# Kernel tuning notes

Measured on AMD Instinct MI355X. Metric: run time of the kernel, lower is better.

Reference implementation:

```python
import jax, jax.numpy as jnp
import numpy as np

EPS_LN = 1e-5
EPS_VAR = 1e-4
GAMMA = 1.0
H, D = 8, 64  # heads, dim_head
DIM = 512
QG, N = 8, 1024  # query groups, tokens


def layernorm(x, g, b):
    mu = x.mean(-1, keepdims=True)
    var = ((x - mu) ** 2).mean(-1, keepdims=True)
    return (x - mu) * jax.lax.rsqrt(var + EPS_LN) * g + b


def setup_inputs() -> dict:
    key = jax.random.key(0)
    ks = jax.random.split(key, 12)
    s_in = 1.0 / np.sqrt(DIM)
    s_p1 = 1.0 / np.sqrt(2 * D)
    s_p2 = 1.0 / np.sqrt(D)
    return {
        "q": jax.random.normal(ks[0], (QG, N, DIM), jnp.float32),
        "k": jax.random.normal(ks[1], (QG, N, DIM), jnp.float32),
        "v": jax.random.normal(ks[2], (QG, N, DIM), jnp.float32),
        "ln_g": jnp.ones((DIM,), jnp.float32),
        "ln_b": jnp.zeros((DIM,), jnp.float32),
        "w_in": jax.random.uniform(ks[3], (DIM, H * D), jnp.float32, -s_in, s_in),
        "p_w1": jax.random.uniform(ks[4], (2 * D, D), jnp.float32, -s_p1, s_p1),
        "p_b1": jax.random.uniform(ks[5], (D,), jnp.float32, -s_p1, s_p1),
        "p_ln_g": jnp.ones((D,), jnp.float32),
        "p_ln_b": jnp.zeros((D,), jnp.float32),
        "p_w2": jax.random.uniform(ks[6], (D, 1), jnp.float32, -s_p2, s_p2),
        "p_b2": jax.random.uniform(ks[7], (1,), jnp.float32, -s_p2, s_p2),
        "w_out": jax.random.uniform(ks[8], (H * D, DIM), jnp.float32, -s_in, s_in),
        "b_out": jax.random.uniform(ks[9], (DIM,), jnp.float32, -s_in, s_in),
    }


def variance_term(E):
    flat = E.reshape(-1, E.shape[-1])  # [h*q*n, d]
    std = jnp.sqrt(jnp.var(flat, axis=0, ddof=1) + EPS_VAR)
    return jnp.maximum(GAMMA - std, 0.0).mean()


def reference(q, k, v, ln_g, ln_b, w_in, p_w1, p_b1, p_ln_g, p_ln_b, p_w2, p_b2, w_out, b_out):
    def proj(t):
        x = layernorm(t, ln_g, ln_b) @ w_in  # [q, n, h*d]
        return jnp.transpose(x.reshape(QG, N, H, D), (2, 0, 1, 3))  # [h, q, n, d]

    f_q, f_k, f_v = proj(q), proj(k), proj(v)

    # cosine-distance scores
    dots = jnp.einsum("hqnd,hqmd->hqnm", f_q, f_k)
    nq = jnp.linalg.norm(f_q, axis=-1)  # [h, q, n]
    nk = jnp.linalg.norm(f_k, axis=-1)  # [h, q, n]
    cos = dots / (nq[..., :, None] * nk[..., None, :])

    # covariance scores (mean-centered over feature dim)
    q_c = f_q - f_q.mean(-1, keepdims=True)
    k_c = f_k - f_k.mean(-1, keepdims=True)
    cov = jnp.einsum("hqnd,hqmd->hqnm", q_c, k_c) / D

    # dynamic per-head mixing weight via small MLP gate
    v_pen = variance_term(f_q) + variance_term(f_k)
    qg = f_q.mean((1, 2))  # [h, d]
    kg = f_k.mean((1, 2))  # [h, d]
    x = jnp.concatenate([qg, kg], -1)  # [h, 2d]
    h1 = jax.nn.relu(layernorm(x @ p_w1 + p_b1, p_ln_g, p_ln_b))
    w = jax.nn.sigmoid(h1 @ p_w2 + p_b2)  # [h, 1]
    w = (w / (1.0 + v_pen)).reshape(H, 1, 1, 1)

    mixed = (1.0 - w) * cos + w * cov  # [h, q, n, n] (no softmax)
    out = jnp.einsum("hqnm,hqmd->hqnd", mixed, f_v)
    out = jnp.transpose(out, (1, 2, 0, 3)).reshape(QG, N, H * D)  # 'h q n d -> q n (h d)'
    return out @ w_out + b_out
```

## Files before the change

### kernel.cpp

```cpp
#include <hip/hip_runtime.h>
#include <cstdint>


typedef unsigned short u16;
typedef unsigned int u32;
typedef __attribute__((ext_vector_type(8))) unsigned short u16x8;
typedef __attribute__((ext_vector_type(4))) unsigned short u16x4;
typedef __attribute__((ext_vector_type(8))) short short8;
typedef __attribute__((ext_vector_type(4))) float floatx4;

#define WS_XBF     0LL
#define WS_OATT    4194304LL
#define WS_WPT     6291456LL
#define WS_WOT     6422528LL
#define WS_U       6553600LL
#define WS_CB      6554112LL
#define WS_LNST    6554624LL
#define WS_FQ      6603776LL
#define WS_FKTS    8700928LL
#define WS_FKTC    10798080LL
#define WS_FVT     12895232LL
#define WS_INVNQ   14992384LL
#define WS_INVNK   15057920LL
#define WS_QMEAN   15123456LL
#define WS_KMEAN   15188992LL
#define WS_COLP    15254528LL
#define WS_WGATE   15385600LL
#define WS_WTF32   15385664LL
#define WS_GSUM    15385664LL
#define WS_MTB     15385664LL
#define WS_CTB     15516736LL
#define WS_COLC    15647808LL

__device__ __forceinline__ float wsum(float v) {
#pragma unroll
    for (int m = 32; m; m >>= 1) v += __shfl_xor(v, m, 64);
    return v;
}
__device__ __forceinline__ u16 f2bf(float f) {
    u32 u = __float_as_uint(f);
    u32 r = u + 0x7fffu + ((u >> 16) & 1u);
    return (u16)(r >> 16);
}
__device__ __forceinline__ float bf2f(u16 u) {
    return __uint_as_float(((u32)u) << 16);
}

__global__ __launch_bounds__(256) void k_lnstats(
    const float* __restrict__ q, const float* __restrict__ k,
    const float* __restrict__ v, float* __restrict__ ws) {
    int wid = threadIdx.x >> 6, lane = threadIdx.x & 63;
    int row = blockIdx.x * 4 + wid;
    int t = row >> 13, r = row & 8191;
    const float* src = (t == 0) ? q : ((t == 1) ? k : v);
    const float4* p = (const float4*)(src + (size_t)r * 512) + lane * 2;
    float4 a = p[0], b = p[1];
    u16x8 o;
    o[0] = f2bf(a.x); o[1] = f2bf(a.y); o[2] = f2bf(a.z); o[3] = f2bf(a.w);
    o[4] = f2bf(b.x); o[5] = f2bf(b.y); o[6] = f2bf(b.z); o[7] = f2bf(b.w);
    *(u16x8*)((u16*)(ws + WS_XBF) + (size_t)row * 512 + lane * 8) = o;
    float s = a.x + a.y + a.z + a.w + b.x + b.y + b.z + b.w;
    float ss = a.x * a.x + a.y * a.y + a.z * a.z + a.w * a.w +
               b.x * b.x + b.y * b.y + b.z * b.z + b.w * b.w;
    s = wsum(s); ss = wsum(ss);
    if (lane == 0) {
        float mu = s * (1.f / 512.f);
        float var = ss * (1.f / 512.f) - mu * mu;
        ws[WS_LNST + (size_t)row * 2] = mu;
        ws[WS_LNST + (size_t)row * 2 + 1] = rsqrtf(var + 1e-5f);
    }
}

template <int SCALE>
__global__ __launch_bounds__(256) void k_prep_t(
    const float* __restrict__ W, const float* __restrict__ g,
    u16* __restrict__ Tb, float* __restrict__ Tf) {
    __shared__ float tile[64][65];
    int k0 = blockIdx.x * 64, j0 = blockIdx.y * 64;
    int tid = threadIdx.x;
    int c = (tid & 15) * 4, r0 = tid >> 4;
#pragma unroll
    for (int p = 0; p < 4; p++) {
        int r = r0 + p * 16;
        *(float4*)&tile[r][c] = *(const float4*)(W + (size_t)(k0 + r) * 512 + j0 + c);
    }
    __syncthreads();
    int kc = (tid & 15) * 4, jr0 = tid >> 4;
#pragma unroll
    for (int p = 0; p < 4; p++) {
        int jr = jr0 + p * 16;
        float v0 = tile[kc + 0][jr], v1 = tile[kc + 1][jr];
        float v2 = tile[kc + 2][jr], v3 = tile[kc + 3][jr];
        if (SCALE) {
            *(float4*)(Tf + (size_t)(j0 + jr) * 512 + k0 + kc) = (float4){v0, v1, v2, v3};
            v0 *= g[k0 + kc + 0]; v1 *= g[k0 + kc + 1];
            v2 *= g[k0 + kc + 2]; v3 *= g[k0 + kc + 3];
        }
        u16x4 ob = {f2bf(v0), f2bf(v1), f2bf(v2), f2bf(v3)};
        *(u16x4*)(Tb + (size_t)(j0 + jr) * 512 + k0 + kc) = ob;
    }
}

__global__ __launch_bounds__(256) void k_prep_u(
    const float* __restrict__ g, const float* __restrict__ b, float* __restrict__ ws) {
    int wid = threadIdx.x >> 6, lane = threadIdx.x & 63;
    int j = blockIdx.x * 4 + wid;
    const float* Tf = ws + WS_WTF32 + (size_t)j * 512;
    float su = 0.f, sc = 0.f;
#pragma unroll
    for (int m = 0; m < 8; m++) {
        int k = lane * 8 + m;
        float w = Tf[k];
        su += g[k] * w; sc += b[k] * w;
    }
    su = wsum(su); sc = wsum(sc);
    if (lane == 0) { ws[WS_U + j] = su; ws[WS_CB + j] = sc; }
}

template <int CPX>
__global__ __launch_bounds__(512, 2) void k_proj(
    const u16* __restrict__ A, const u16* __restrict__ B, float* __restrict__ ws) {
    __shared__ char smem[131072];
    int tid = threadIdx.x;
    int wid = tid >> 6, lane = tid & 63;
    int i15 = lane & 15, q4 = lane >> 4;
    int wm = wid >> 2, wn = wid & 3;
    int flat = blockIdx.x + (blockIdx.y << 2);
    int swz = (flat & 7) * CPX + (flat >> 3);
    int c0 = (swz & 3) * 128, m0 = (swz >> 2) * 128;

    floatx4 acc[3][4][2];
#pragma unroll
    for (int t = 0; t < 3; t++)
#pragma unroll
        for (int i = 0; i < 4; i++)
#pragma unroll
            for (int j = 0; j < 2; j++) acc[t][i][j] = (floatx4){0.f, 0.f, 0.f, 0.f};

    const u16* gB = B + (size_t)c0 * 512;

    auto stage = [&](int ks, int buf) {
        int o = wid * 1024 + lane * 16;
        int srow = o >> 6, s = (o >> 4) & 3;
        int cch = (s - (srow >> 1)) & 3;
        size_t roff = (size_t)srow * 512 + ks * 32 + cch * 8;
        char* base = smem + buf * 32768 + wid * 1024;
#pragma unroll
        for (int t = 0; t < 3; t++) {
            const u16* ga = A + (size_t)(t * 8192 + m0) * 512 + roff;
            __builtin_amdgcn_global_load_lds(
                (const __attribute__((address_space(1))) void*)ga,
                (__attribute__((address_space(3))) void*)(base + t * 8192), 16, 0, 0);
        }
        __builtin_amdgcn_global_load_lds(
            (const __attribute__((address_space(1))) void*)(gB + roff),
            (__attribute__((address_space(3))) void*)(base + 24576), 16, 0, 0);
    };

    stage(0, 0);
    stage(1, 1);
    stage(2, 2);
    __builtin_amdgcn_sched_barrier(0);
#pragma unroll
    for (int ks = 0; ks < 16; ks++) {
        __builtin_amdgcn_sched_barrier(0);
        if (ks <= 13)      asm volatile("s_waitcnt vmcnt(8)" ::: "memory");
        else if (ks == 14) asm volatile("s_waitcnt vmcnt(4)" ::: "memory");
        else               asm volatile("s_waitcnt vmcnt(0)" ::: "memory");
        __builtin_amdgcn_s_barrier();
        __builtin_amdgcn_sched_barrier(0);
        if (ks + 3 < 16) stage(ks + 3, (ks + 3) & 3);
        __builtin_amdgcn_sched_barrier(0);
        char* bb = smem + (ks & 3) * 32768;
        short8 b[2];
#pragma unroll
        for (int f = 0; f < 2; f++) {
            int rb = wn * 32 + f * 16 + i15;
            int sb = (q4 + (rb >> 1)) & 3;
            b[f] = *(const short8*)(bb + 24576 + rb * 64 + sb * 16);
        }
#pragma unroll
        for (int t = 0; t < 3; t++) {
            short8 a[4];
#pragma unroll
            for (int f = 0; f < 4; f++) {
                int ra = wm * 64 + f * 16 + i15;
                int sa = (q4 + (ra >> 1)) & 3;
                a[f] = *(const short8*)(bb + t * 8192 + ra * 64 + sa * 16);
            }
#pragma unroll
            for (int fm = 0; fm < 4; fm++)
#pragma unroll
                for (int fn = 0; fn < 2; fn++)
                    acc[t][fm][fn] = __builtin_amdgcn_mfma_f32_16x16x32_bf16(
                        a[fm], b[fn], acc[t][fm][fn], 0, 0, 0);
        }
    }

    float2* rowred = (float2*)smem;
    float2* colred = (float2*)(smem + 4096);
    float2* lnfin  = (float2*)(smem + 6144);
    int nbase = m0 & 1023;
    int qg = m0 >> 10, nblk = (m0 >> 7) & 7;
    int hp = wn >> 1;
    int h = (c0 >> 6) + hp, hq = h * 8 + qg;
    int dwn = (wn & 1) * 32;
    float u_[2], cb_[2];
#pragma unroll
    for (int fn = 0; fn < 2; fn++) {
        int gc = c0 + wn * 32 + fn * 16 + i15;
        u_[fn] = ws[WS_U + gc]; cb_[fn] = ws[WS_CB + gc];
    }
#pragma unroll
    for (int t = 0; t < 3; t++) {
        __syncthreads();
        float csum[2] = {0, 0}, css[2] = {0, 0};
#pragma unroll
        for (int fm = 0; fm < 4; fm++) {
#pragma unroll
            for (int reg = 0; reg < 4; reg++) {
                int grow = t * 8192 + m0 + wm * 64 + fm * 16 + q4 * 4 + reg;
                float2 st = *(const float2*)(ws + WS_LNST + (size_t)grow * 2);
                float mu = st.x, rs = st.y;
                float r1 = 0.f, r2 = 0.f;
#pragma unroll
                for (int fn = 0; fn < 2; fn++) {
                    float val = rs * acc[t][fm][fn][reg] - rs * mu * u_[fn] + cb_[fn];
                    acc[t][fm][fn][reg] = val;
                    r1 += val; r2 += val * val;
                    csum[fn] += val; css[fn] += val * val;
                }
                if (t < 2) {
#pragma unroll
                    for (int m = 1; m < 16; m <<= 1) {
                        r1 += __shfl_xor(r1, m, 64);
                        r2 += __shfl_xor(r2, m, 64);
                    }
                    if (i15 == fm * 4 + reg)
                        rowred[(size_t)wid * 64 + fm * 16 + q4 * 4 + reg] = (float2){r1, r2};
                }
            }
        }
        if (t < 2) {
#pragma unroll
            for (int fn = 0; fn < 2; fn++) {
                float s1 = csum[fn], s2 = css[fn];
                s1 += __shfl_xor(s1, 16, 64); s1 += __shfl_xor(s1, 32, 64);
                s2 += __shfl_xor(s2, 16, 64); s2 += __shfl_xor(s2, 32, 64);
                if (q4 == fn) colred[(size_t)wid * 32 + fn * 16 + i15] = (float2){s1, s2};
            }
        }
        __syncthreads();
        if (t < 2) {
            float* invn = ws + (t ? WS_INVNK : WS_INVNQ);
            float* mean = ws + (t ? WS_KMEAN : WS_QMEAN);
            if (tid < 256) {
                int wmf = tid >> 7, p = (tid >> 6) & 1, r = tid & 63;
                float2 aa = rowred[(size_t)(wmf * 4 + 2 * p) * 64 + r];
                float2 bb2 = rowred[(size_t)(wmf * 4 + 2 * p + 1) * 64 + r];
                float s1 = aa.x + bb2.x, s2 = aa.y + bb2.y;
                float iv = rsqrtf(s2), mn = s1 * (1.f / 64.f);
                int n = nbase + wmf * 64 + r;
                int hhq = ((c0 >> 6) + p) * 8 + qg;
                invn[(size_t)hhq * 1024 + n] = iv;
                mean[(size_t)hhq * 1024 + n] = mn;
                lnfin[p * 128 + wmf * 64 + r] = (float2){iv, mn};
            } else if (tid < 384) {
                int tt = tid - 256;
                int p = tt >> 6, d = tt & 63;
                int wnn = 2 * p + (d >> 5), loc = d & 31;
                float2 aa = colred[(size_t)(0 * 4 + wnn) * 32 + loc];
                float2 bb2 = colred[(size_t)(1 * 4 + wnn) * 32 + loc];
                int hhq = ((c0 >> 6) + p) * 8 + qg;
                *(float2*)(ws + WS_COLP +
                           (size_t)(((t * 64 + hhq) * 8 + nblk) * 64 + d) * 2) =
                    (float2){aa.x + bb2.x, aa.y + bb2.y};
            }
        }
        __syncthreads();
        if (t == 0) {
            u16* fout = (u16*)(ws + WS_FQ) + (size_t)hq * 65536;
#pragma unroll
            for (int fm = 0; fm < 4; fm++)
#pragma unroll
                for (int reg = 0; reg < 4; reg++) {
                    int n = nbase + wm * 64 + fm * 16 + q4 * 4 + reg;
#pragma unroll
                    for (int fn = 0; fn < 2; fn++)
                        fout[(size_t)n * 64 + dwn + fn * 16 + i15] =
                            f2bf(acc[0][fm][fn][reg]);
                }
        } else if (t == 1) {
            u16* fs = (u16*)(ws + WS_FKTS) + (size_t)hq * 65536;
            u16* fc = (u16*)(ws + WS_FKTC) + (size_t)hq * 65536;
#pragma unroll
            for (int fn = 0; fn < 2; fn++) {
                int eoff = ((wn & 1) * 2 + fn) * 16384 + i15 * 32;
#pragma unroll
                for (int fm = 0; fm < 4; fm++) {
                    int n0l = wm * 64 + fm * 16 + q4 * 4;
                    int n0 = nbase + n0l;
                    int off = eoff + (n0 >> 5) * 512 + ((n0 >> 3) & 3) * 8 + (n0 & 7);
                    u16x4 vs, vc;
#pragma unroll
                    for (int reg = 0; reg < 4; reg++) {
                        float2 im = lnfin[hp * 128 + n0l + reg];
                        float val = acc[1][fm][fn][reg];
                        vs[reg] = f2bf(val * im.x);
                        vc[reg] = f2bf(val - im.y);
                    }
                    *(u16x4*)(fs + off) = vs;
                    *(u16x4*)(fc + off) = vc;
                }
            }
        } else {
            u16* fv = (u16*)(ws + WS_FVT) + (size_t)hq * 65536;
#pragma unroll
            for (int fn = 0; fn < 2; fn++) {
                int doff = ((wn & 1) * 2 + fn) * 16384 + i15 * 32;
#pragma unroll
                for (int fm = 0; fm < 4; fm++) {
                    int n0 = nbase + wm * 64 + fm * 16 + q4 * 4;
                    int off = doff + (n0 >> 5) * 512 + ((n0 >> 3) & 3) * 8 + (n0 & 7);
                    u16x4 v4;
#pragma unroll
                    for (int reg = 0; reg < 4; reg++) v4[reg] = f2bf(acc[2][fm][fn][reg]);
                    *(u16x4*)(fv + off) = v4;
                }
            }
        }
    }
}

template <int CPX>
__global__ __launch_bounds__(512, 4) void k_gemm_out(
    const u16* __restrict__ A, const u16* __restrict__ B,
    float* __restrict__ out, const float* __restrict__ bias) {
    __shared__ char smem[65536];
    int tid = threadIdx.x;
    int wid = tid >> 6, lane = tid & 63;
    int i15 = lane & 15, q4 = lane >> 4;
    int wm = wid >> 2, wn = wid & 3;
    int flat = blockIdx.x + (blockIdx.y << 2);
    int swz = (flat & 7) * CPX + (flat >> 3);
    int c0 = (swz & 3) * 128, m0 = (swz >> 2) * 128;

    floatx4 acc[4][2];
#pragma unroll
    for (int i = 0; i < 4; i++)
#pragma unroll
        for (int j = 0; j < 2; j++) acc[i][j] = (floatx4){0.f, 0.f, 0.f, 0.f};

    const u16* gA = A + (size_t)m0 * 512;
    const u16* gB = B + (size_t)c0 * 512;

    auto stage = [&](int ks, int buf) {
        int o = wid * 1024 + lane * 16;
        int srow = o >> 6, s = (o >> 4) & 3;
        int cch = (s - (srow >> 1)) & 3;
        const u16* ga = gA + (size_t)srow * 512 + ks * 32 + cch * 8;
        const u16* gb = gB + (size_t)srow * 512 + ks * 32 + cch * 8;
        char* la = smem + buf * 16384 + wid * 1024;
        char* lb = smem + buf * 16384 + 8192 + wid * 1024;
        __builtin_amdgcn_global_load_lds(
            (const __attribute__((address_space(1))) void*)ga,
            (__attribute__((address_space(3))) void*)la, 16, 0, 0);
        __builtin_amdgcn_global_load_lds(
            (const __attribute__((address_space(1))) void*)gb,
            (__attribute__((address_space(3))) void*)lb, 16, 0, 0);
    };

    stage(0, 0);
    stage(1, 1);
    stage(2, 2);
    __builtin_amdgcn_sched_barrier(0);
#pragma unroll
    for (int ks = 0; ks < 16; ks++) {
        __builtin_amdgcn_sched_barrier(0);
        if (ks <= 13)      asm volatile("s_waitcnt vmcnt(4)" ::: "memory");
        else if (ks == 14) asm volatile("s_waitcnt vmcnt(2)" ::: "memory");
        else               asm volatile("s_waitcnt vmcnt(0)" ::: "memory");
        __builtin_amdgcn_s_barrier();
        __builtin_amdgcn_sched_barrier(0);
        if (ks + 3 < 16) stage(ks + 3, (ks + 3) & 3);
        __builtin_amdgcn_sched_barrier(0);
        int buf = ks & 3;
        short8 a[4], b[2];
#pragma unroll
        for (int f = 0; f < 4; f++) {
            int ra = wm * 64 + f * 16 + i15;
            int sa = (q4 + (ra >> 1)) & 3;
            a[f] = *(const short8*)(smem + buf * 16384 + ra * 64 + sa * 16);
        }
#pragma unroll
        for (int f = 0; f < 2; f++) {
            int rb = wn * 32 + f * 16 + i15;
            int sb = (q4 + (rb >> 1)) & 3;
            b[f] = *(const short8*)(smem + buf * 16384 + 8192 + rb * 64 + sb * 16);
        }
#pragma unroll
        for (int fm = 0; fm < 4; fm++)
#pragma unroll
            for (int fn = 0; fn < 2; fn++)
                acc[fm][fn] = __builtin_amdgcn_mfma_f32_16x16x32_bf16(
                    a[fm], b[fn], acc[fm][fn], 0, 0, 0);
    }
#pragma unroll
    for (int fm = 0; fm < 4; fm++)
#pragma unroll
        for (int reg = 0; reg < 4; reg++) {
            int gm = m0 + wm * 64 + fm * 16 + q4 * 4 + reg;
#pragma unroll
            for (int fn = 0; fn < 2; fn++) {
                int gc = c0 + wn * 32 + fn * 16 + i15;
                out[(size_t)gm * 512 + gc] = acc[fm][fn][reg] + bias[gc];
            }
        }
}

__global__ __launch_bounds__(256) void k_gatered(float* __restrict__ ws) {
    int h = blockIdx.x, t = blockIdx.y;
    int tid = threadIdx.x;
    int c = tid & 127, rg = tid >> 7;
    const float* base = ws + WS_COLP + ((size_t)(t * 64 + h * 8) * 8) * 128;
    float s = 0.f;
#pragma unroll 8
    for (int r = rg * 32; r < rg * 32 + 32; r++) s += base[(size_t)r * 128 + c];
    __shared__ float red[2][128];
    red[rg][c] = s;
    __syncthreads();
    if (tid < 128)
        ws[WS_GSUM + ((size_t)t * 8 + h) * 128 + tid] = red[0][tid] + red[1][tid];
}

__global__ __launch_bounds__(256) void k_gate(
    const float* __restrict__ pw1, const float* __restrict__ pb1,
    const float* __restrict__ plg, const float* __restrict__ plb,
    const float* __restrict__ pw2, const float* __restrict__ pb2,
    float* __restrict__ ws) {
    __shared__ float w1[128][64];
    __shared__ float gs[2][8][128];
    int tid = threadIdx.x, wid = tid >> 6, lane = tid & 63;
    for (int r = wid; r < 128; r += 4) w1[r][lane] = pw1[r * 64 + lane];
    for (int i = tid; i < 2048; i += 256) ((float*)gs)[i] = ws[WS_GSUM + i];
    __syncthreads();
    if (wid != 0) return;
    float Sq = 0, SSq = 0, Sk = 0, SSk = 0;
#pragma unroll
    for (int h = 0; h < 8; h++) {
        Sq += gs[0][h][lane * 2];  SSq += gs[0][h][lane * 2 + 1];
        Sk += gs[1][h][lane * 2];  SSk += gs[1][h][lane * 2 + 1];
    }
    const float NR = 65536.f;
    float stdq = sqrtf((SSq - Sq * Sq / NR) / (NR - 1.f) + 1e-4f);
    float stdk = sqrtf((SSk - Sk * Sk / NR) / (NR - 1.f) + 1e-4f);
    float vpen = (wsum(fmaxf(1.f - stdq, 0.f)) + wsum(fmaxf(1.f - stdk, 0.f))) * (1.f / 64.f);
    float gammav = plg[lane], betav = plb[lane], w2v = pw2[lane];
    for (int h = 0; h < 8; h++) {
        float y = pb1[lane];
#pragma unroll 8
        for (int i = 0; i < 64; i++) {
            y = fmaf(gs[0][h][i * 2] * (1.f / 8192.f), w1[i][lane], y);
            y = fmaf(gs[1][h][i * 2] * (1.f / 8192.f), w1[64 + i][lane], y);
        }
        float mu = wsum(y) * (1.f / 64.f);
        float dv = y - mu;
        float var = wsum(dv * dv) * (1.f / 64.f);
        float z = dv * rsqrtf(var + 1e-5f) * gammav + betav;
        float r = fmaxf(z, 0.f);
        float sdot = wsum(r * w2v);
        if (lane == 0) {
            float wv = 1.f / (1.f + expf(-(sdot + pb2[0])));
            ws[WS_WGATE + h] = wv / (1.f + vpen);
        }
    }
}

__global__ __launch_bounds__(256) void k_mc(float* __restrict__ ws) {
    int hq = blockIdx.x;
    int tid = threadIdx.x, wid = tid >> 6, lane = tid & 63;
    int i15 = lane & 15, q4 = lane >> 4;
    int we = wid >> 1, wd = wid & 1;
    const u16* fs = (const u16*)(ws + WS_FKTS) + (size_t)hq * 65536;
    const u16* fc = (const u16*)(ws + WS_FKTC) + (size_t)hq * 65536;
    const u16* fv = (const u16*)(ws + WS_FVT) + (size_t)hq * 65536;
    floatx4 aM[2][2], aC[2][2];
#pragma unroll
    for (int f = 0; f < 2; f++)
#pragma unroll
        for (int g = 0; g < 2; g++) {
            aM[f][g] = (floatx4){0.f, 0.f, 0.f, 0.f};
            aC[f][g] = (floatx4){0.f, 0.f, 0.f, 0.f};
        }
#pragma unroll 8
    for (int ks = 0; ks < 32; ks++) {
        short8 as_[2], ac_[2], b_[2];
#pragma unroll
        for (int f = 0; f < 2; f++) {
            int off = (we * 2 + f) * 16384 + ks * 512 + i15 * 32 + q4 * 8;
            as_[f] = *(const short8*)(fs + off);
            ac_[f] = *(const short8*)(fc + off);
        }
#pragma unroll
        for (int g = 0; g < 2; g++)
            b_[g] = *(const short8*)(fv + (wd * 2 + g) * 16384 + ks * 512 +
                                     i15 * 32 + q4 * 8);
#pragma unroll
        for (int f = 0; f < 2; f++)
#pragma unroll
            for (int g = 0; g < 2; g++) {
                aM[f][g] = __builtin_amdgcn_mfma_f32_16x16x32_bf16(
                    as_[f], b_[g], aM[f][g], 0, 0, 0);
                aC[f][g] = __builtin_amdgcn_mfma_f32_16x16x32_bf16(
                    ac_[f], b_[g], aC[f][g], 0, 0, 0);
            }
    }
    __shared__ float tile[2][64][65];
    __shared__ float cred[4][64];
#pragma unroll
    for (int f = 0; f < 2; f++)
#pragma unroll
        for (int g = 0; g < 2; g++)
#pragma unroll
            for (int reg = 0; reg < 4; reg++) {
                int e = we * 32 + f * 16 + q4 * 4 + reg;
                int d = wd * 32 + g * 16 + i15;
                tile[0][e][d] = aM[f][g][reg];
                tile[1][e][d] = aC[f][g][reg];
            }
    __syncthreads();
    int d = tid & 63, ec = tid >> 6;
    float cp = 0.f;
#pragma unroll
    for (int i = 0; i < 16; i++) cp += tile[1][ec * 16 + i][d];
    cred[ec][d] = cp;
#pragma unroll
    for (int mat = 0; mat < 2; mat++) {
        u16x8 p0, p1;
#pragma unroll
        for (int i = 0; i < 8; i++) {
            p0[i] = f2bf(tile[mat][ec * 16 + i][d]);
            p1[i] = f2bf(tile[mat][ec * 16 + 8 + i][d]);
        }
        u16* dst = (u16*)(ws + (mat ? WS_CTB : WS_MTB)) + (size_t)hq * 4096 + d * 64 + ec * 16;
        *(u16x8*)dst = p0;
        *(u16x8*)(dst + 8) = p1;
    }
    __syncthreads();
    if (tid < 64)
        ws[WS_COLC + (size_t)hq * 64 + tid] =
            cred[0][tid] + cred[1][tid] + cred[2][tid] + cred[3][tid];
}

__global__ __launch_bounds__(256) void k_apply(float* __restrict__ ws) {
    int nt = blockIdx.x, hq = blockIdx.y;
    int h = hq >> 3, qg = hq & 7;
    __shared__ u16 mt[2][4096];
    __shared__ float invqm[256][2];
    __shared__ u16 outs[256][66];
    int tid = threadIdx.x, wid = tid >> 6, lane = tid & 63;
    int i15 = lane & 15, q4 = lane >> 4;
#pragma unroll
    for (int mat = 0; mat < 2; mat++) {
        const u16* src = (const u16*)(ws + (mat ? WS_CTB : WS_MTB)) + (size_t)hq * 4096;
#pragma unroll
        for (int it = 0; it < 2; it++) {
            int i = tid + it * 256;
            int d = i >> 3, c8 = i & 7;
            u16x8 v = *(const u16x8*)(src + i * 8);
            int byte = d * 128 + ((c8 * 16) ^ ((d & 7) << 4));
            *(u16x8*)((char*)&mt[mat][0] + byte) = v;
        }
    }
    int R0 = nt * 256;
    invqm[tid][0] = ws[WS_INVNQ + (size_t)hq * 1024 + R0 + tid];
    invqm[tid][1] = ws[WS_QMEAN + (size_t)hq * 1024 + R0 + tid];
    float wv = ws[WS_WGATE + h];
    float c1 = 1.f - wv, c2 = wv * (1.f / 64.f);
    float colc[4];
#pragma unroll
    for (int fn = 0; fn < 4; fn++)
        colc[fn] = ws[WS_COLC + (size_t)hq * 64 + fn * 16 + i15];
    __syncthreads();
    const u16* fq = (const u16*)(ws + WS_FQ) + (size_t)hq * 65536 +
                    (size_t)(R0 + wid * 64) * 64;
    floatx4 aM[4][4], aC[4][4];
#pragma unroll
    for (int i = 0; i < 4; i++)
#pragma unroll
        for (int j = 0; j < 4; j++) {
            aM[i][j] = (floatx4){0.f, 0.f, 0.f, 0.f};
            aC[i][j] = (floatx4){0.f, 0.f, 0.f, 0.f};
        }
#pragma unroll
    for (int ks = 0; ks < 2; ks++) {
        short8 a[4], bM[4], bC[4];
#pragma unroll
        for (int f = 0; f < 4; f++)
            a[f] = *(const short8*)(fq + (size_t)(f * 16 + i15) * 64 + q4 * 8 + ks * 32);
#pragma unroll
        for (int f = 0; f < 4; f++) {
            int col = f * 16 + i15;
            int byte = col * 128 + ((q4 * 16 + ks * 64) ^ ((col & 7) << 4));
            bM[f] = *(const short8*)((char*)&mt[0][0] + byte);
            bC[f] = *(const short8*)((char*)&mt[1][0] + byte);
        }
#pragma unroll
        for (int fm = 0; fm < 4; fm++)
#pragma unroll
            for (int fn = 0; fn < 4; fn++) {
                aM[fm][fn] = __builtin_amdgcn_mfma_f32_16x16x32_bf16(
                    a[fm], bM[fn], aM[fm][fn], 0, 0, 0);
                aC[fm][fn] = __builtin_amdgcn_mfma_f32_16x16x32_bf16(
                    a[fm], bC[fn], aC[fm][fn], 0, 0, 0);
            }
    }
#pragma unroll
    for (int fm = 0; fm < 4; fm++)
#pragma unroll
        for (int reg = 0; reg < 4; reg++) {
            int rloc = wid * 64 + fm * 16 + q4 * 4 + reg;
            float iv = invqm[rloc][0], qmv = invqm[rloc][1];
#pragma unroll
            for (int fn = 0; fn < 4; fn++) {
                float val = c1 * iv * aM[fm][fn][reg] +
                            c2 * (aC[fm][fn][reg] - qmv * colc[fn]);
                outs[rloc][fn * 16 + i15] = f2bf(val);
            }
        }
    __syncthreads();
    u16* oat = (u16*)(ws + WS_OATT);
#pragma unroll
    for (int it = 0; it < 8; it++) {
        int c = tid + it * 256;
        int row = c >> 3, c8 = (c & 7) * 8;
        u16x8 v = *(const u16x8*)&outs[row][c8];
        *(u16x8*)(oat + ((size_t)qg * 1024 + R0 + row) * 512 + h * 64 + c8) = v;
    }
}

extern "C" void kernel_launch(void* const* d_in, const int* in_sizes, int n_in,
                              void* d_out, int out_size, void* d_ws, size_t ws_size,
                              hipStream_t stream) {
    (void)in_sizes; (void)n_in; (void)out_size; (void)ws_size;
    const float* q = (const float*)d_in[0];
    const float* k = (const float*)d_in[1];
    const float* v = (const float*)d_in[2];
    const float* ln_g = (const float*)d_in[3];
    const float* ln_b = (const float*)d_in[4];
    const float* w_in = (const float*)d_in[5];
    const float* p_w1 = (const float*)d_in[6];
    const float* p_b1 = (const float*)d_in[7];
    const float* p_ln_g = (const float*)d_in[8];
    const float* p_ln_b = (const float*)d_in[9];
    const float* p_w2 = (const float*)d_in[10];
    const float* p_b2 = (const float*)d_in[11];
    const float* w_out = (const float*)d_in[12];
    const float* b_out = (const float*)d_in[13];
    float* ws = (float*)d_ws;
    float* out = (float*)d_out;

    k_lnstats<<<6144, 256, 0, stream>>>(q, k, v, ws);
    k_prep_t<1><<<dim3(8, 8), 256, 0, stream>>>(w_in, ln_g, (u16*)(ws + WS_WPT), ws + WS_WTF32);
    k_prep_t<0><<<dim3(8, 8), 256, 0, stream>>>(w_out, nullptr, (u16*)(ws + WS_WOT), nullptr);
    k_prep_u<<<128, 256, 0, stream>>>(ln_g, ln_b, ws);
    k_proj<32><<<dim3(4, 64), 512, 0, stream>>>((const u16*)(ws + WS_XBF),
                                                (const u16*)(ws + WS_WPT), ws);
    k_gatered<<<dim3(8, 2), 256, 0, stream>>>(ws);
    k_gate<<<1, 256, 0, stream>>>(p_w1, p_b1, p_ln_g, p_ln_b, p_w2, p_b2, ws);
    k_mc<<<64, 256, 0, stream>>>(ws);
    k_apply<<<dim3(4, 64), 256, 0, stream>>>(ws);
    k_gemm_out<32><<<dim3(4, 64), 512, 0, stream>>>((const u16*)(ws + WS_OATT),
                                                    (const u16*)(ws + WS_WOT), out, b_out);
}
```

Measured before the change: 115.8 us.

## Split projection GEMM into Q/K and V blocks to raise occupancy, merge weight prep

The fused projection kernel, which computed Q, K and V tiles together, is split across twice as many blocks. Half handle Q and K, the other half handle V alone. The LDS footprint shrinks to triple-buffered 24KB stages and the launch bounds rise to 4 blocks per SM, aiming for more parallelism and latency hiding. The two weight-transpose prep launches become one launch with a z-dimension to save launch overhead. The trade-off is more blocks re-reading the same B tiles, and a shallower prefetch depth of 2 instead of 3.

After: 124.0 us. +7.0%, slower.

```diff
diff --git a/kernel.cpp b/kernel.cpp
--- a/kernel.cpp
+++ b/kernel.cpp
@@ -71,11 +71,14 @@
     }
 }
 
-template <int SCALE>
-__global__ __launch_bounds__(256) void k_prep_t(
-    const float* __restrict__ W, const float* __restrict__ g,
-    u16* __restrict__ Tb, float* __restrict__ Tf) {
+__global__ __launch_bounds__(256) void k_prep(
+    const float* __restrict__ Wa, const float* __restrict__ Wb,
+    const float* __restrict__ g, float* __restrict__ ws) {
     __shared__ float tile[64][65];
+    int which = blockIdx.z;
+    const float* W = which ? Wb : Wa;
+    u16* Tb = (u16*)(ws + (which ? WS_WOT : WS_WPT));
+    float* Tf = ws + WS_WTF32;
     int k0 = blockIdx.x * 64, j0 = blockIdx.y * 64;
     int tid = threadIdx.x;
     int c = (tid & 15) * 4, r0 = tid >> 4;
@@ -91,7 +94,7 @@
         int jr = jr0 + p * 16;
         float v0 = tile[kc + 0][jr], v1 = tile[kc + 1][jr];
         float v2 = tile[kc + 2][jr], v3 = tile[kc + 3][jr];
-        if (SCALE) {
+        if (which == 0) {
             *(float4*)(Tf + (size_t)(j0 + jr) * 512 + k0 + kc) = (float4){v0, v1, v2, v3};
             v0 *= g[k0 + kc + 0]; v1 *= g[k0 + kc + 1];
             v2 *= g[k0 + kc + 2]; v3 *= g[k0 + kc + 3];
@@ -118,84 +121,23 @@
 }
 
 template <int CPX>
-__global__ __launch_bounds__(512, 2) void k_proj(
+__global__ __launch_bounds__(512, 4) void k_proj(
     const u16* __restrict__ A, const u16* __restrict__ B, float* __restrict__ ws) {
-    __shared__ char smem[131072];
+    __shared__ char smem[73728];
     int tid = threadIdx.x;
     int wid = tid >> 6, lane = tid & 63;
     int i15 = lane & 15, q4 = lane >> 4;
     int wm = wid >> 2, wn = wid & 3;
-    int flat = blockIdx.x + (blockIdx.y << 2);
+    int isv = (blockIdx.x >= 256);
+    int flat = blockIdx.x - (isv ? 256 : 0);
     int swz = (flat & 7) * CPX + (flat >> 3);
     int c0 = (swz & 3) * 128, m0 = (swz >> 2) * 128;
 
-    floatx4 acc[3][4][2];
-#pragma unroll
-    for (int t = 0; t < 3; t++)
-#pragma unroll
-        for (int i = 0; i < 4; i++)
-#pragma unroll
-            for (int j = 0; j < 2; j++) acc[t][i][j] = (floatx4){0.f, 0.f, 0.f, 0.f};
-
     const u16* gB = B + (size_t)c0 * 512;
-
-    auto stage = [&](int ks, int buf) {
-        int o = wid * 1024 + lane * 16;
-        int srow = o >> 6, s = (o >> 4) & 3;
-        int cch = (s - (srow >> 1)) & 3;
-        size_t roff = (size_t)srow * 512 + ks * 32 + cch * 8;
-        char* base = smem + buf * 32768 + wid * 1024;
-#pragma unroll
-        for (int t = 0; t < 3; t++) {
-            const u16* ga = A + (size_t)(t * 8192 + m0) * 512 + roff;
-            __builtin_amdgcn_global_load_lds(
-                (const __attribute__((address_space(1))) void*)ga,
-                (__attribute__((address_space(3))) void*)(base + t * 8192), 16, 0, 0);
-        }
-        __builtin_amdgcn_global_load_lds(
-            (const __attribute__((address_space(1))) void*)(gB + roff),
-            (__attribute__((address_space(3))) void*)(base + 24576), 16, 0, 0);
-    };
-
-    stage(0, 0);
-    stage(1, 1);
-    stage(2, 2);
-    __builtin_amdgcn_sched_barrier(0);
-#pragma unroll
-    for (int ks = 0; ks < 16; ks++) {
-        __builtin_amdgcn_sched_barrier(0);
-        if (ks <= 13)      asm volatile("s_waitcnt vmcnt(8)" ::: "memory");
-        else if (ks == 14) asm volatile("s_waitcnt vmcnt(4)" ::: "memory");
-        else               asm volatile("s_waitcnt vmcnt(0)" ::: "memory");
-        __builtin_amdgcn_s_barrier();
-        __builtin_amdgcn_sched_barrier(0);
-        if (ks + 3 < 16) stage(ks + 3, (ks + 3) & 3);
-        __builtin_amdgcn_sched_barrier(0);
-        char* bb = smem + (ks & 3) * 32768;
-        short8 b[2];
-#pragma unroll
-        for (int f = 0; f < 2; f++) {
-            int rb = wn * 32 + f * 16 + i15;
-            int sb = (q4 + (rb >> 1)) & 3;
-            b[f] = *(const short8*)(bb + 24576 + rb * 64 + sb * 16);
-        }
-#pragma unroll
-        for (int t = 0; t < 3; t++) {
-            short8 a[4];
-#pragma unroll
-            for (int f = 0; f < 4; f++) {
-                int ra = wm * 64 + f * 16 + i15;
-                int sa = (q4 + (ra >> 1)) & 3;
-                a[f] = *(const short8*)(bb + t * 8192 + ra * 64 + sa * 16);
-            }
-#pragma unroll
-            for (int fm = 0; fm < 4; fm++)
-#pragma unroll
-                for (int fn = 0; fn < 2; fn++)
-                    acc[t][fm][fn] = __builtin_amdgcn_mfma_f32_16x16x32_bf16(
-                        a[fm], b[fn], acc[t][fm][fn], 0, 0, 0);
-        }
-    }
+    int o = wid * 1024 + lane * 16;
+    int srow = o >> 6, s8 = (o >> 4) & 3;
+    int cch = (s8 - (srow >> 1)) & 3;
+    size_t roffb = (size_t)srow * 512 + cch * 8;
 
     float2* rowred = (float2*)smem;
     float2* colred = (float2*)(smem + 4096);
@@ -205,32 +147,93 @@
     int hp = wn >> 1;
     int h = (c0 >> 6) + hp, hq = h * 8 + qg;
     int dwn = (wn & 1) * 32;
-    float u_[2], cb_[2];
-#pragma unroll
-    for (int fn = 0; fn < 2; fn++) {
-        int gc = c0 + wn * 32 + fn * 16 + i15;
-        u_[fn] = ws[WS_U + gc]; cb_[fn] = ws[WS_CB + gc];
-    }
-#pragma unroll
-    for (int t = 0; t < 3; t++) {
-        __syncthreads();
-        float csum[2] = {0, 0}, css[2] = {0, 0};
-#pragma unroll
-        for (int fm = 0; fm < 4; fm++) {
-#pragma unroll
-            for (int reg = 0; reg < 4; reg++) {
-                int grow = t * 8192 + m0 + wm * 64 + fm * 16 + q4 * 4 + reg;
-                float2 st = *(const float2*)(ws + WS_LNST + (size_t)grow * 2);
-                float mu = st.x, rs = st.y;
-                float r1 = 0.f, r2 = 0.f;
-#pragma unroll
-                for (int fn = 0; fn < 2; fn++) {
-                    float val = rs * acc[t][fm][fn][reg] - rs * mu * u_[fn] + cb_[fn];
-                    acc[t][fm][fn][reg] = val;
-                    r1 += val; r2 += val * val;
-                    csum[fn] += val; css[fn] += val * val;
+
+    if (!isv) {
+        floatx4 acc[2][4][2];
+#pragma unroll
+        for (int t = 0; t < 2; t++)
+#pragma unroll
+            for (int i = 0; i < 4; i++)
+#pragma unroll
+                for (int j = 0; j < 2; j++) acc[t][i][j] = (floatx4){0.f, 0.f, 0.f, 0.f};
+
+        auto stage = [&](int ks, int buf) {
+            size_t roff = roffb + ks * 32;
+            char* base = smem + buf * 24576 + wid * 1024;
+            __builtin_amdgcn_global_load_lds(
+                (const __attribute__((address_space(1))) void*)(A + (size_t)m0 * 512 + roff),
+                (__attribute__((address_space(3))) void*)(base), 16, 0, 0);
+            __builtin_amdgcn_global_load_lds(
+                (const __attribute__((address_space(1))) void*)(A + (size_t)(8192 + m0) * 512 + roff),
+                (__attribute__((address_space(3))) void*)(base + 8192), 16, 0, 0);
+            __builtin_amdgcn_global_load_lds(
+                (const __attribute__((address_space(1))) void*)(gB + roff),
+                (__attribute__((address_space(3))) void*)(base + 16384), 16, 0, 0);
+        };
+
+        stage(0, 0);
+        stage(1, 1);
+        __builtin_amdgcn_sched_barrier(0);
+#pragma unroll
+        for (int ks = 0; ks < 16; ks++) {
+            __builtin_amdgcn_sched_barrier(0);
+            if (ks <= 14) asm volatile("s_waitcnt vmcnt(3)" ::: "memory");
+            else          asm volatile("s_waitcnt vmcnt(0)" ::: "memory");
+            __builtin_amdgcn_s_barrier();
+            __builtin_amdgcn_sched_barrier(0);
+            if (ks + 2 < 16) stage(ks + 2, (ks + 2) % 3);
+            __builtin_amdgcn_sched_barrier(0);
+            char* bb = smem + (ks % 3) * 24576;
+            short8 b[2];
+#pragma unroll
+            for (int f = 0; f < 2; f++) {
+                int rb = wn * 32 + f * 16 + i15;
+                int sb = (q4 + (rb >> 1)) & 3;
+                b[f] = *(const short8*)(bb + 16384 + rb * 64 + sb * 16);
+            }
+#pragma unroll
+            for (int t = 0; t < 2; t++) {
+                short8 a[4];
+#pragma unroll
+                for (int f = 0; f < 4; f++) {
+                    int ra = wm * 64 + f * 16 + i15;
+                    int sa = (q4 + (ra >> 1)) & 3;
+                    a[f] = *(const short8*)(bb + t * 8192 + ra * 64 + sa * 16);
                 }
-                if (t < 2) {
+#pragma unroll
+                for (int fm = 0; fm < 4; fm++)
+#pragma unroll
+                    for (int fn = 0; fn < 2; fn++)
+                        acc[t][fm][fn] = __builtin_amdgcn_mfma_f32_16x16x32_bf16(
+                            a[fm], b[fn], acc[t][fm][fn], 0, 0, 0);
+            }
+        }
+
+        float u_[2], cb_[2];
+#pragma unroll
+        for (int fn = 0; fn < 2; fn++) {
+            int gc = c0 + wn * 32 + fn * 16 + i15;
+            u_[fn] = ws[WS_U + gc]; cb_[fn] = ws[WS_CB + gc];
+        }
+#pragma unroll
+        for (int t = 0; t < 2; t++) {
+            __syncthreads();
+            float csum[2] = {0, 0}, css[2] = {0, 0};
+#pragma unroll
+            for (int fm = 0; fm < 4; fm++) {
+#pragma unroll
+                for (int reg = 0; reg < 4; reg++) {
+                    int grow = t * 8192 + m0 + wm * 64 + fm * 16 + q4 * 4 + reg;
+                    float2 st = *(const float2*)(ws + WS_LNST + (size_t)grow * 2);
+                    float mu = st.x, rs = st.y;
+                    float r1 = 0.f, r2 = 0.f;
+#pragma unroll
+                    for (int fn = 0; fn < 2; fn++) {
+                        float val = rs * acc[t][fm][fn][reg] - rs * mu * u_[fn] + cb_[fn];
+                        acc[t][fm][fn][reg] = val;
+                        r1 += val; r2 += val * val;
+                        csum[fn] += val; css[fn] += val * val;
+                    }
 #pragma unroll
                     for (int m = 1; m < 16; m <<= 1) {
                         r1 += __shfl_xor(r1, m, 64);
@@ -240,8 +243,6 @@
                         rowred[(size_t)wid * 64 + fm * 16 + q4 * 4 + reg] = (float2){r1, r2};
                 }
             }
-        }
-        if (t < 2) {
 #pragma unroll
             for (int fn = 0; fn < 2; fn++) {
                 float s1 = csum[fn], s2 = css[fn];
@@ -249,84 +250,147 @@
                 s2 += __shfl_xor(s2, 16, 64); s2 += __shfl_xor(s2, 32, 64);
                 if (q4 == fn) colred[(size_t)wid * 32 + fn * 16 + i15] = (float2){s1, s2};
             }
-        }
-        __syncthreads();
-        if (t < 2) {
-            float* invn = ws + (t ? WS_INVNK : WS_INVNQ);
-            float* mean = ws + (t ? WS_KMEAN : WS_QMEAN);
-            if (tid < 256) {
-                int wmf = tid >> 7, p = (tid >> 6) & 1, r = tid & 63;
-                float2 aa = rowred[(size_t)(wmf * 4 + 2 * p) * 64 + r];
-                float2 bb2 = rowred[(size_t)(wmf * 4 + 2 * p + 1) * 64 + r];
-                float s1 = aa.x + bb2.x, s2 = aa.y + bb2.y;
-                float iv = rsqrtf(s2), mn = s1 * (1.f / 64.f);
-                int n = nbase + wmf * 64 + r;
-                int hhq = ((c0 >> 6) + p) * 8 + qg;
-                invn[(size_t)hhq * 1024 + n] = iv;
-                mean[(size_t)hhq * 1024 + n] = mn;
-                lnfin[p * 128 + wmf * 64 + r] = (float2){iv, mn};
-            } else if (tid < 384) {
-                int tt = tid - 256;
-                int p = tt >> 6, d = tt & 63;
-                int wnn = 2 * p + (d >> 5), loc = d & 31;
-                float2 aa = colred[(size_t)(0 * 4 + wnn) * 32 + loc];
-                float2 bb2 = colred[(size_t)(1 * 4 + wnn) * 32 + loc];
-                int hhq = ((c0 >> 6) + p) * 8 + qg;
-                *(float2*)(ws + WS_COLP +
-                           (size_t)(((t * 64 + hhq) * 8 + nblk) * 64 + d) * 2) =
-                    (float2){aa.x + bb2.x, aa.y + bb2.y};
-            }
-        }
-        __syncthreads();
-        if (t == 0) {
-            u16* fout = (u16*)(ws + WS_FQ) + (size_t)hq * 65536;
+            __syncthreads();
+            {
+                float* invn = ws + (t ? WS_INVNK : WS_INVNQ);
+                float* mean = ws + (t ? WS_KMEAN : WS_QMEAN);
+                if (tid < 256) {
+                    int wmf = tid >> 7, p = (tid >> 6) & 1, r = tid & 63;
+                    float2 aa = rowred[(size_t)(wmf * 4 + 2 * p) * 64 + r];
+                    float2 bb2 = rowred[(size_t)(wmf * 4 + 2 * p + 1) * 64 + r];
+                    float s1 = aa.x + bb2.x, s2 = aa.y + bb2.y;
+                    float iv = rsqrtf(s2), mn = s1 * (1.f / 64.f);
+                    int n = nbase + wmf * 64 + r;
+                    int hhq = ((c0 >> 6) + p) * 8 + qg;
+                    invn[(size_t)hhq * 1024 + n] = iv;
+                    mean[(size_t)hhq * 1024 + n] = mn;
+                    lnfin[p * 128 + wmf * 64 + r] = (float2){iv, mn};
+                } else if (tid < 384) {
+                    int tt = tid - 256;
+                    int p = tt >> 6, d = tt & 63;
+                    int wnn = 2 * p + (d >> 5), loc = d & 31;
+                    float2 aa = colred[(size_t)(0 * 4 + wnn) * 32 + loc];
+                    float2 bb2 = colred[(size_t)(1 * 4 + wnn) * 32 + loc];
+                    int hhq = ((c0 >> 6) + p) * 8 + qg;
+                    *(float2*)(ws + WS_COLP +
+                               (size_t)(((t * 64 + hhq) * 8 + nblk) * 64 + d) * 2) =
+                        (float2){aa.x + bb2.x, aa.y + bb2.y};
+                }
+            }
+            __syncthreads();
+            if (t == 0) {
+                u16* fout = (u16*)(ws + WS_FQ) + (size_t)hq * 65536;
+#pragma unroll
+                for (int fm = 0; fm < 4; fm++)
+#pragma unroll
+                    for (int reg = 0; reg < 4; reg++) {
+                        int n = nbase + wm * 64 + fm * 16 + q4 * 4 + reg;
+#pragma unroll
+                        for (int fn = 0; fn < 2; fn++)
+                            fout[(size_t)n * 64 + dwn + fn * 16 + i15] =
+                                f2bf(acc[0][fm][fn][reg]);
+                    }
+            } else {
+                u16* fs = (u16*)(ws + WS_FKTS) + (size_t)hq * 65536;
+                u16* fc = (u16*)(ws + WS_FKTC) + (size_t)hq * 65536;
+#pragma unroll
+                for (int fn = 0; fn < 2; fn++) {
+                    int eoff = ((wn & 1) * 2 + fn) * 16384 + i15 * 32;
+#pragma unroll
+                    for (int fm = 0; fm < 4; fm++) {
+                        int n0l = wm * 64 + fm * 16 + q4 * 4;
+                        int n0 = nbase + n0l;
+                        int off = eoff + (n0 >> 5) * 512 + ((n0 >> 3) & 3) * 8 + (n0 & 7);
+                        u16x4 vs, vc;
+#pragma unroll
+                        for (int reg = 0; reg < 4; reg++) {
+                            float2 im = lnfin[hp * 128 + n0l + reg];
+                            float val = acc[1][fm][fn][reg];
+                            vs[reg] = f2bf(val * im.x);
+                            vc[reg] = f2bf(val - im.y);
+                        }
+                        *(u16x4*)(fs + off) = vs;
+                        *(u16x4*)(fc + off) = vc;
+                    }
+                }
+            }
+        }
+    } else {
+        floatx4 acc[4][2];
+#pragma unroll
+        for (int i = 0; i < 4; i++)
+#pragma unroll
+            for (int j = 0; j < 2; j++) acc[i][j] = (floatx4){0.f, 0.f, 0.f, 0.f};
+
+        auto stage = [&](int ks, int buf) {
+            size_t roff = roffb + ks * 32;
+            char* base = smem + buf * 24576 + wid * 1024;
+            __builtin_amdgcn_global_load_lds(
+                (const __attribute__((address_space(1))) void*)(A + (size_t)(16384 + m0) * 512 + roff),
+                (__attribute__((address_space(3))) void*)(base), 16, 0, 0);
+            __builtin_amdgcn_global_load_lds(
+                (const __attribute__((address_space(1))) void*)(gB + roff),
+                (__attribute__((address_space(3))) void*)(base + 8192), 16, 0, 0);
+        };
+
+        stage(0, 0);
+        stage(1, 1);
+        __builtin_amdgcn_sched_barrier(0);
+#pragma unroll
+        for (int ks = 0; ks < 16; ks++) {
+            __builtin_amdgcn_sched_barrier(0);
+            if (ks <= 14) asm volatile("s_waitcnt vmcnt(2)" ::: "memory");
+            else          asm volatile("s_waitcnt vmcnt(0)" ::: "memory");
+            __builtin_amdgcn_s_barrier();
+            __builtin_amdgcn_sched_barrier(0);
+            if (ks + 2 < 16) stage(ks + 2, (ks + 2) % 3);
+            __builtin_amdgcn_sched_barrier(0);
+            char* bb = smem + (ks % 3) * 24576;
+            short8 a[4], b[2];
+#pragma unroll
+            for (int f = 0; f < 4; f++) {
+                int ra = wm * 64 + f * 16 + i15;
+                int sa = (q4 + (ra >> 1)) & 3;
+                a[f] = *(const short8*)(bb + ra * 64 + sa * 16);
+            }
+#pragma unroll
+            for (int f = 0; f < 2; f++) {
+                int rb = wn * 32 + f * 16 + i15;
+                int sb = (q4 + (rb >> 1)) & 3;
+                b[f] = *(const short8*)(bb + 8192 + rb * 64 + sb * 16);
+            }
 #pragma unroll
             for (int fm = 0; fm < 4; fm++)
 #pragma unroll
+                for (int fn = 0; fn < 2; fn++)
+                    acc[fm][fn] = __builtin_amdgcn_mfma_f32_16x16x32_bf16(
+                        a[fm], b[fn], acc[fm][fn], 0, 0, 0);
+        }
+
+        float u_[2], cb_[2];
+#pragma unroll
+        for (int fn = 0; fn < 2; fn++) {
+            int gc = c0 + wn * 32 + fn * 16 + i15;
+            u_[fn] = ws[WS_U + gc]; cb_[fn] = ws[WS_CB + gc];
+        }
+        u16* fv = (u16*)(ws + WS_FVT) + (size_t)hq * 65536;
+#pragma unroll
+        for (int fn = 0; fn < 2; fn++) {
+            int doff = ((wn & 1) * 2 + fn) * 16384 + i15 * 32;
+#pragma unroll
+            for (int fm = 0; fm < 4; fm++) {
+                int n0l = wm * 64 + fm * 16 + q4 * 4;
+                int n0 = nbase + n0l;
+                int off = doff + (n0 >> 5) * 512 + ((n0 >> 3) & 3) * 8 + (n0 & 7);
+                u16x4 v4;
+#pragma unroll
                 for (int reg = 0; reg < 4; reg++) {
-                    int n = nbase + wm * 64 + fm * 16 + q4 * 4 + reg;
-#pragma unroll
-                    for (int fn = 0; fn < 2; fn++)
-                        fout[(size_t)n * 64 + dwn + fn * 16 + i15] =
-                            f2bf(acc[0][fm][fn][reg]);
+                    int grow = 16384 + m0 + n0l - (n0l) + wm * 64 + fm * 16 + q4 * 4 + reg;
+                    float2 st = *(const float2*)(ws + WS_LNST + (size_t)grow * 2);
+                    float val = st.y * acc[fm][fn][reg] - st.y * st.x * u_[fn] + cb_[fn];
+                    v4[reg] = f2bf(val);
                 }
-        } else if (t == 1) {
-            u16* fs = (u16*)(ws + WS_FKTS) + (size_t)hq * 65536;
-            u16* fc = (u16*)(ws + WS_FKTC) + (size_t)hq * 65536;
-#pragma unroll
-            for (int fn = 0; fn < 2; fn++) {
-                int eoff = ((wn & 1) * 2 + fn) * 16384 + i15 * 32;
-#pragma unroll
-                for (int fm = 0; fm < 4; fm++) {
-                    int n0l = wm * 64 + fm * 16 + q4 * 4;
-                    int n0 = nbase + n0l;
-                    int off = eoff + (n0 >> 5) * 512 + ((n0 >> 3) & 3) * 8 + (n0 & 7);
-                    u16x4 vs, vc;
-#pragma unroll
-                    for (int reg = 0; reg < 4; reg++) {
-                        float2 im = lnfin[hp * 128 + n0l + reg];
-                        float val = acc[1][fm][fn][reg];
-                        vs[reg] = f2bf(val * im.x);
-                        vc[reg] = f2bf(val - im.y);
-                    }
-                    *(u16x4*)(fs + off) = vs;
-                    *(u16x4*)(fc + off) = vc;
-                }
-            }
-        } else {
-            u16* fv = (u16*)(ws + WS_FVT) + (size_t)hq * 65536;
-#pragma unroll
-            for (int fn = 0; fn < 2; fn++) {
-                int doff = ((wn & 1) * 2 + fn) * 16384 + i15 * 32;
-#pragma unroll
-                for (int fm = 0; fm < 4; fm++) {
-                    int n0 = nbase + wm * 64 + fm * 16 + q4 * 4;
-                    int off = doff + (n0 >> 5) * 512 + ((n0 >> 3) & 3) * 8 + (n0 & 7);
-                    u16x4 v4;
-#pragma unroll
-                    for (int reg = 0; reg < 4; reg++) v4[reg] = f2bf(acc[2][fm][fn][reg]);
-                    *(u16x4*)(fv + off) = v4;
-                }
+                *(u16x4*)(fv + off) = v4;
             }
         }
     }
@@ -661,11 +725,10 @@
     float* out = (float*)d_out;
 
     k_lnstats<<<6144, 256, 0, stream>>>(q, k, v, ws);
-    k_prep_t<1><<<dim3(8, 8), 256, 0, stream>>>(w_in, ln_g, (u16*)(ws + WS_WPT), ws + WS_WTF32);
-    k_prep_t<0><<<dim3(8, 8), 256, 0, stream>>>(w_out, nullptr, (u16*)(ws + WS_WOT), nullptr);
+    k_prep<<<dim3(8, 8, 2), 256, 0, stream>>>(w_in, w_out, ln_g, ws);
     k_prep_u<<<128, 256, 0, stream>>>(ln_g, ln_b, ws);
-    k_proj<32><<<dim3(4, 64), 512, 0, stream>>>((const u16*)(ws + WS_XBF),
-                                                (const u16*)(ws + WS_WPT), ws);
+    k_proj<32><<<512, 512, 0, stream>>>((const u16*)(ws + WS_XBF),
+                                        (const u16*)(ws + WS_WPT), ws);
     k_gatered<<<dim3(8, 2), 256, 0, stream>>>(ws);
     k_gate<<<1, 256, 0, stream>>>(p_w1, p_b1, p_ln_g, p_ln_b, p_w2, p_b2, ws);
     k_mc<<<64, 256, 0, stream>>>(ws);
```
